# Performance work log

Hardware: AMD Instinct MI355X
Metric: run time of the kernel (lower is better)

Reference implementation:

```python
import jax, jax.numpy as jnp
import numpy as np

N_NODES = 50000
IN_CH = 128
OUT_CH = 64
HEADS = 2
N_EDGES = 400000
NEG_SLOPE = 0.2  # PyG GATConv default


def _glorot(key, shape):
    fan_in, fan_out = shape[0], shape[-1]
    lim = jnp.sqrt(6.0 / (fan_in + fan_out))
    return jax.random.uniform(key, shape, jnp.float32, -lim, lim)


def setup_inputs() -> dict:
    key = jax.random.key(0)
    ks = jax.random.split(key, 12)
    hid = 2 * OUT_CH  # per-head channels of conv1
    inp = {
        "x": jax.random.normal(ks[0], (N_NODES, IN_CH), jnp.float32),
        "edge_index": jax.random.randint(ks[1], (2, N_EDGES), 0, N_NODES, jnp.int32),
        # conv1: in=IN_CH, out=hid per head, HEADS heads, concat
        "W1": _glorot(ks[2], (IN_CH, HEADS * hid)),
        "att_src1": _glorot(ks[3], (HEADS, hid)),
        "att_dst1": _glorot(ks[4], (HEADS, hid)),
        "b1": jnp.zeros((HEADS * hid,), jnp.float32),
        # conv_mu: in=hid*HEADS, out=OUT_CH, 1 head
        "W_mu": _glorot(ks[5], (hid * HEADS, OUT_CH)),
        "att_src_mu": _glorot(ks[6], (1, OUT_CH)),
        "att_dst_mu": _glorot(ks[7], (1, OUT_CH)),
        "b_mu": jnp.zeros((OUT_CH,), jnp.float32),
        # conv_logstd: same shapes as conv_mu
        "W_ls": _glorot(ks[8], (hid * HEADS, OUT_CH)),
        "att_src_ls": _glorot(ks[9], (1, OUT_CH)),
        "att_dst_ls": _glorot(ks[10], (1, OUT_CH)),
        "b_ls": jnp.zeros((OUT_CH,), jnp.float32),
    }
    return inp


def gat_conv(x, src, dst, W, att_src, att_dst, b, n_nodes):
    """PyG GATConv (add_self_loops handled by caller in src/dst)."""
    H, C = att_src.shape
    h = (x @ W).reshape(n_nodes, H, C)                       # [N,H,C]
    a_src = jnp.einsum('nhc,hc->nh', h, att_src)             # [N,H]
    a_dst = jnp.einsum('nhc,hc->nh', h, att_dst)
    e = jax.nn.leaky_relu(a_src[src] + a_dst[dst], NEG_SLOPE)  # [E,H]
    # scatter-softmax over incoming edges per destination node
    m = jax.ops.segment_max(e, dst, num_segments=n_nodes)
    e = jnp.exp(e - m[dst])
    denom = jax.ops.segment_sum(e, dst, num_segments=n_nodes)
    alpha = e / (denom[dst] + 1e-16)                          # [E,H]
    out = jax.ops.segment_sum(h[src] * alpha[:, :, None], dst,
                              num_segments=n_nodes)           # [N,H,C]
    return out.reshape(n_nodes, H * C) + b


def reference(x, edge_index, W1, att_src1, att_dst1, b1,
              W_mu, att_src_mu, att_dst_mu, b_mu,
              W_ls, att_src_ls, att_dst_ls, b_ls):
    n = x.shape[0]
    loop = jnp.arange(n, dtype=edge_index.dtype)
    src = jnp.concatenate([edge_index[0], loop])  # add self-loops (PyG default)
    dst = jnp.concatenate([edge_index[1], loop])
    h = jax.nn.elu(gat_conv(x, src, dst, W1, att_src1, att_dst1, b1, n))
    mu = gat_conv(h, src, dst, W_mu, att_src_mu, att_dst_mu, b_mu, n)
    logstd = gat_conv(h, src, dst, W_ls, att_src_ls, att_dst_ls, b_ls, n)
    return (mu, logstd)
```

## Files before the change

kernel.cpp:

```cpp
#include <hip/hip_runtime.h>
#include <math.h>

#define N_NODES 50000
#define N_EDGES 400000
#define PAD 64

typedef __attribute__((ext_vector_type(8))) short bf16x8;
typedef __attribute__((ext_vector_type(4))) float f32x4;

__device__ __forceinline__ float lrelu(float x){ return x > 0.f ? x : 0.2f*x; }
__device__ __forceinline__ float bf2f(unsigned short u){ return __uint_as_float(((unsigned int)u)<<16); }
__device__ __forceinline__ unsigned short f2bf(float f){
    unsigned int b = __float_as_uint(f);
    return (unsigned short)((b + 0x7FFFu + ((b>>16)&1u)) >> 16);
}
__device__ __forceinline__ float4 bf4(ushort4 u){
    return make_float4(bf2f(u.x), bf2f(u.y), bf2f(u.z), bf2f(u.w));
}
__device__ __forceinline__ float wexp(float e){ return __expf(fminf(e, 80.f)); }

__global__ __launch_bounds__(256) void vprep_k(const float* __restrict__ W1,
        const float* __restrict__ attS, const float* __restrict__ attD,
        float* __restrict__ V1){
    int t = threadIdx.x;
    for (int idx = t; idx < 512; idx += 256){
        int v = idx >> 7, k = idx & 127;
        int h = v & 1;
        const float* attp = (v >> 1) ? attD : attS;
        float s = 0.f;
        #pragma unroll 8
        for (int c = 0; c < 128; c++)
            s = fmaf(W1[k*256 + h*128 + c], attp[h*128 + c], s);
        V1[idx] = s;
    }
}

__global__ __launch_bounds__(256) void prep_k(const float* __restrict__ x, unsigned short* __restrict__ xb,
        const float* __restrict__ V1, float2* __restrict__ as1, float2* __restrict__ ad1,
        const float* __restrict__ W1, const float* __restrict__ Wmu, const float* __restrict__ Wls,
        unsigned short* __restrict__ W1T, unsigned short* __restrict__ WmlT,
        const int* __restrict__ src, const int* __restrict__ dst,
        int* __restrict__ counts, int* __restrict__ csr_src){
    int t = threadIdx.x;
    int gthr = blockIdx.x*256 + t;

    int n = blockIdx.x*4 + (t >> 6);
    int lane = t & 63;
    if (n < N_NODES){
        int c0 = lane*2;
        float2 xv = ((const float2*)(x + (size_t)n*128))[lane];
        ((ushort2*)(xb + (size_t)n*128))[lane] = make_ushort2(f2bf(xv.x), f2bf(xv.y));
        float s0 = xv.x*V1[      c0] + xv.y*V1[      c0+1];
        float s1 = xv.x*V1[128 + c0] + xv.y*V1[128 + c0+1];
        float d0 = xv.x*V1[256 + c0] + xv.y*V1[256 + c0+1];
        float d1 = xv.x*V1[384 + c0] + xv.y*V1[384 + c0+1];
        #pragma unroll
        for (int m = 1; m < 64; m <<= 1){
            s0 += __shfl_xor(s0, m);
            s1 += __shfl_xor(s1, m);
            d0 += __shfl_xor(d0, m);
            d1 += __shfl_xor(d1, m);
        }
        if (lane == 0){
            as1[n] = make_float2(s0, s1);
            ad1[n] = make_float2(d0, d1);
        }
    }

    if (gthr < 32768){
        int i = gthr;
        int nn = i >> 7, k = i & 127;
        W1T[i] = f2bf(W1[k*256 + nn]);
        int n2 = i >> 8, k2 = i & 255;
        float v = (n2 < 64) ? Wmu[k2*64 + n2] : Wls[k2*64 + (n2-64)];
        WmlT[i] = f2bf(v);
    }

    if (gthr < N_EDGES){
        int d = dst[gthr];
        int pos = atomicAdd(&counts[d], 1);
        csr_src[d*PAD + pos] = src[gthr];
    }
}

__global__ __launch_bounds__(256) void agg1x_k(const unsigned short* __restrict__ xb,
        const float2* __restrict__ as, const float2* __restrict__ ad,
        const int* __restrict__ counts, const int* __restrict__ csr_src,
        unsigned short* __restrict__ aggx0, unsigned short* __restrict__ aggx1){
    int wave = threadIdx.x >> 6, lane = threadIdx.x & 63;
    int n = blockIdx.x*4 + wave;
    if (n >= N_NODES) return;

    float2 adn = ad[n], asn = as[n];
    float w0s = wexp(lrelu(asn.x + adn.x));
    float w1s = wexp(lrelu(asn.y + adn.y));
    float l0 = w0s, l1 = w1s;

    ushort2 u = ((const ushort2*)(xb + (size_t)n*128))[lane];
    float rx = bf2f(u.x), ry = bf2f(u.y);
    float a0x = w0s*rx, a0y = w0s*ry;
    float a1x = w1s*rx, a1y = w1s*ry;

    int deg = counts[n];
    int off = n*PAD;
    int dm1 = deg - 1;
    for (int k = 0; k < deg; k += 4){
        int s0 = csr_src[off + k];
        int s1 = csr_src[off + min(k+1, dm1)];
        int s2 = csr_src[off + min(k+2, dm1)];
        int s3 = csr_src[off + min(k+3, dm1)];
        float2 e0 = as[s0], e1 = as[s1], e2 = as[s2], e3 = as[s3];
        ushort2 u0 = ((const ushort2*)(xb + (size_t)s0*128))[lane];
        ushort2 u1 = ((const ushort2*)(xb + (size_t)s1*128))[lane];
        ushort2 u2 = ((const ushort2*)(xb + (size_t)s2*128))[lane];
        ushort2 u3 = ((const ushort2*)(xb + (size_t)s3*128))[lane];
        float w00 = wexp(lrelu(e0.x + adn.x));
        float w01 = wexp(lrelu(e0.y + adn.y));
        float w10 = (k+1 <= dm1) ? wexp(lrelu(e1.x + adn.x)) : 0.f;
        float w11 = (k+1 <= dm1) ? wexp(lrelu(e1.y + adn.y)) : 0.f;
        float w20 = (k+2 <= dm1) ? wexp(lrelu(e2.x + adn.x)) : 0.f;
        float w21 = (k+2 <= dm1) ? wexp(lrelu(e2.y + adn.y)) : 0.f;
        float w30 = (k+3 <= dm1) ? wexp(lrelu(e3.x + adn.x)) : 0.f;
        float w31 = (k+3 <= dm1) ? wexp(lrelu(e3.y + adn.y)) : 0.f;
        l0 += (w00 + w10) + (w20 + w30);
        l1 += (w01 + w11) + (w21 + w31);
        float r0x = bf2f(u0.x), r0y = bf2f(u0.y);
        float r1x = bf2f(u1.x), r1y = bf2f(u1.y);
        float r2x = bf2f(u2.x), r2y = bf2f(u2.y);
        float r3x = bf2f(u3.x), r3y = bf2f(u3.y);
        a0x = fmaf(w00, r0x, a0x); a0y = fmaf(w00, r0y, a0y);
        a1x = fmaf(w01, r0x, a1x); a1y = fmaf(w01, r0y, a1y);
        a0x = fmaf(w10, r1x, a0x); a0y = fmaf(w10, r1y, a0y);
        a1x = fmaf(w11, r1x, a1x); a1y = fmaf(w11, r1y, a1y);
        a0x = fmaf(w20, r2x, a0x); a0y = fmaf(w20, r2y, a0y);
        a1x = fmaf(w21, r2x, a1x); a1y = fmaf(w21, r2y, a1y);
        a0x = fmaf(w30, r3x, a0x); a0y = fmaf(w30, r3y, a0y);
        a1x = fmaf(w31, r3x, a1x); a1y = fmaf(w31, r3y, a1y);
    }

    float i0 = 1.f / (l0 + 1e-16f);
    float i1 = 1.f / (l1 + 1e-16f);
    ((ushort2*)(aggx0 + (size_t)n*128))[lane] = make_ushort2(f2bf(a0x*i0), f2bf(a0y*i0));
    ((ushort2*)(aggx1 + (size_t)n*128))[lane] = make_ushort2(f2bf(a1x*i1), f2bf(a1y*i1));
}

template<int MODE>
__global__ __launch_bounds__(256) void mfma_gemm_k(const unsigned short* __restrict__ A0,
        const unsigned short* __restrict__ A1,
        const unsigned short* __restrict__ BT, unsigned short* __restrict__ C,
        int M, int K, int ldc, const float* __restrict__ bias,
        const float* __restrict__ attS0, const float* __restrict__ attD0,
        const float* __restrict__ attS1, const float* __restrict__ attD1,
        float* __restrict__ outS, float* __restrict__ outD){
    __shared__ unsigned short As[128*40];
    __shared__ unsigned short Bs[128*40];
    int t = threadIdx.x;
    int lane = t & 63, wid = t >> 6;
    int wy = wid >> 1, wx = wid & 1;
    int quad = lane >> 4, l15 = lane & 15;
    int row0 = blockIdx.y * 128;
    int col0 = blockIdx.x * 128;
    const unsigned short* A = (MODE == 0 && blockIdx.x) ? A1 : A0;

    f32x4 acc[4][4];
    #pragma unroll
    for (int i = 0; i < 4; i++)
        #pragma unroll
        for (int j = 0; j < 4; j++)
            acc[i][j] = (f32x4){0.f, 0.f, 0.f, 0.f};

    int r = t >> 2;
    int cofs = (t & 3) * 8;

    for (int k0 = 0; k0 < K; k0 += 32){
        int gr0 = min(row0 + r,      M-1);
        int gr1 = min(row0 + r + 64, M-1);
        float4 av0 = *(const float4*)(A  + (size_t)gr0*K + k0 + cofs);
        float4 av1 = *(const float4*)(A  + (size_t)gr1*K + k0 + cofs);
        float4 bv0 = *(const float4*)(BT + (size_t)(col0 + r)*K      + k0 + cofs);
        float4 bv1 = *(const float4*)(BT + (size_t)(col0 + r + 64)*K + k0 + cofs);
        __syncthreads();
        *(float4*)&As[r*40 + cofs]      = av0;
        *(float4*)&As[(r+64)*40 + cofs] = av1;
        *(float4*)&Bs[r*40 + cofs]      = bv0;
        *(float4*)&Bs[(r+64)*40 + cofs] = bv1;
        __syncthreads();

        bf16x8 af[4], bf[4];
        #pragma unroll
        for (int i = 0; i < 4; i++)
            af[i] = *(const bf16x8*)&As[(wy*64 + i*16 + l15)*40 + quad*8];
        #pragma unroll
        for (int j = 0; j < 4; j++)
            bf[j] = *(const bf16x8*)&Bs[(wx*64 + j*16 + l15)*40 + quad*8];
        #pragma unroll
        for (int i = 0; i < 4; i++)
            #pragma unroll
            for (int j = 0; j < 4; j++)
                acc[i][j] = __builtin_amdgcn_mfma_f32_16x16x32_bf16(af[i], bf[j], acc[i][j], 0, 0, 0);
    }

    float aS[4], aD[4], bvals[4];
    #pragma unroll
    for (int j = 0; j < 4; j++){
        int cc = col0 + wx*64 + j*16 + l15;
        if (MODE == 0){
            bvals[j] = bias[cc];
        } else {
            int c2 = j*16 + l15;
            aS[j] = wx ? attS1[c2] : attS0[c2];
            aD[j] = wx ? attD1[c2] : attD0[c2];
        }
    }

    #pragma unroll
    for (int i = 0; i < 4; i++){
        #pragma unroll
        for (int reg = 0; reg < 4; reg++){
            int rr = row0 + wy*64 + i*16 + quad*4 + reg;
            if (MODE == 0){
                if (rr < M){
                    #pragma unroll
                    for (int j = 0; j < 4; j++){
                        int cc = col0 + wx*64 + j*16 + l15;
                        float v = acc[i][j][reg] + bvals[j];
                        v = v > 0.f ? v : __expf(v) - 1.f;
                        C[(size_t)rr*ldc + cc] = f2bf(v);
                    }
                }
            } else {
                float sp = 0.f, dp = 0.f;
                #pragma unroll
                for (int j = 0; j < 4; j++){
                    float v = acc[i][j][reg];
                    int cc = col0 + wx*64 + j*16 + l15;
                    if (rr < M) C[(size_t)rr*ldc + cc] = f2bf(v);
                    sp = fmaf(v, aS[j], sp);
                    dp = fmaf(v, aD[j], dp);
                }
                #pragma unroll
                for (int msk = 1; msk < 16; msk <<= 1){
                    sp += __shfl_xor(sp, msk);
                    dp += __shfl_xor(dp, msk);
                }
                if (l15 == 0 && rr < M){
                    outS[rr*2 + wx] = sp;
                    outD[rr*2 + wx] = dp;
                }
            }
        }
    }
}

__global__ __launch_bounds__(256) void agg2_k(const unsigned short* __restrict__ hml,
        const float* __restrict__ as, const float* __restrict__ ad,
        const int* __restrict__ counts, const int* __restrict__ csr_src,
        const float* __restrict__ b_mu, const float* __restrict__ b_ls,
        float* __restrict__ out){
    int grp = threadIdx.x >> 5, lane = threadIdx.x & 31;
    int n = blockIdx.x*8 + grp;
    if (n >= N_NODES) return;
    int g = lane >> 4;
    const ushort4* hv = (const ushort4*)hml;

    float adh = ad[n*2 + g];
    float ash = as[n*2 + g];

    float w = wexp(lrelu(ash + adh));
    float l = w;
    float4 r = bf4(hv[(size_t)n*32 + lane]);
    float4 acc = make_float4(w*r.x, w*r.y, w*r.z, w*r.w);

    int deg = counts[n];
    int off = n*PAD;
    int dm1 = deg - 1;
    for (int k = 0; k < deg; k += 4){
        int s0 = csr_src[off + k];
        int s1 = csr_src[off + min(k+1, dm1)];
        int s2 = csr_src[off + min(k+2, dm1)];
        int s3 = csr_src[off + min(k+3, dm1)];
        float e0 = as[s0*2 + g], e1 = as[s1*2 + g];
        float e2 = as[s2*2 + g], e3 = as[s3*2 + g];
        float4 r0 = bf4(hv[(size_t)s0*32 + lane]);
        float4 r1 = bf4(hv[(size_t)s1*32 + lane]);
        float4 r2 = bf4(hv[(size_t)s2*32 + lane]);
        float4 r3 = bf4(hv[(size_t)s3*32 + lane]);
        float w0 = wexp(lrelu(e0 + adh));
        float w1 = (k+1 <= dm1) ? wexp(lrelu(e1 + adh)) : 0.f;
        float w2 = (k+2 <= dm1) ? wexp(lrelu(e2 + adh)) : 0.f;
        float w3 = (k+3 <= dm1) ? wexp(lrelu(e3 + adh)) : 0.f;
        l += (w0 + w1) + (w2 + w3);
        acc.x = fmaf(w0, r0.x, acc.x); acc.x = fmaf(w1, r1.x, acc.x);
        acc.x = fmaf(w2, r2.x, acc.x); acc.x = fmaf(w3, r3.x, acc.x);
        acc.y = fmaf(w0, r0.y, acc.y); acc.y = fmaf(w1, r1.y, acc.y);
        acc.y = fmaf(w2, r2.y, acc.y); acc.y = fmaf(w3, r3.y, acc.y);
        acc.z = fmaf(w0, r0.z, acc.z); acc.z = fmaf(w1, r1.z, acc.z);
        acc.z = fmaf(w2, r2.z, acc.z); acc.z = fmaf(w3, r3.z, acc.z);
        acc.w = fmaf(w0, r0.w, acc.w); acc.w = fmaf(w1, r1.w, acc.w);
        acc.w = fmaf(w2, r2.w, acc.w); acc.w = fmaf(w3, r3.w, acc.w);
    }

    float invl = 1.f / (l + 1e-16f);
    int c = (lane & 15) * 4;
    const float* bb = g ? b_ls : b_mu;
    float4 b4 = *(const float4*)&bb[c];
    float4 v;
    v.x = acc.x*invl + b4.x; v.y = acc.y*invl + b4.y;
    v.z = acc.z*invl + b4.z; v.w = acc.w*invl + b4.w;
    float* base = g ? (out + (size_t)N_NODES*64) : out;
    *(float4*)&base[(size_t)n*64 + c] = v;
}

extern "C" void kernel_launch(void* const* d_in, const int* in_sizes, int n_in,
                              void* d_out, int out_size, void* d_ws, size_t ws_size,
                              hipStream_t stream) {
    const float* x           = (const float*)d_in[0];
    const int*   ei          = (const int*)d_in[1];
    const float* W1          = (const float*)d_in[2];
    const float* att_src1    = (const float*)d_in[3];
    const float* att_dst1    = (const float*)d_in[4];
    const float* b1          = (const float*)d_in[5];
    const float* W_mu        = (const float*)d_in[6];
    const float* att_src_mu  = (const float*)d_in[7];
    const float* att_dst_mu  = (const float*)d_in[8];
    const float* b_mu        = (const float*)d_in[9];
    const float* W_ls        = (const float*)d_in[10];
    const float* att_src_ls  = (const float*)d_in[11];
    const float* att_dst_ls  = (const float*)d_in[12];
    const float* b_ls        = (const float*)d_in[13];
    float* out = (float*)d_out;

    const int* srcp = ei;
    const int* dstp = ei + N_EDGES;

    unsigned short* xb    = (unsigned short*)d_ws;
    unsigned short* aggx0 = xb    + (size_t)N_NODES*128;
    unsigned short* aggx1 = aggx0 + (size_t)N_NODES*128;
    unsigned short* hbuf  = aggx1 + (size_t)N_NODES*128;
    unsigned short* hml   = hbuf  + (size_t)N_NODES*256;
    unsigned short* W1T   = hml   + (size_t)N_NODES*128;
    unsigned short* WmlT  = W1T   + 32768;
    int*   counts = (int*)(WmlT + 32768);
    float2* as1   = (float2*)(counts + N_NODES);
    float2* ad1   = as1 + N_NODES;
    float*  as2   = (float*)(ad1 + N_NODES);
    float*  ad2   = as2 + 2*N_NODES;
    float*  V1    = ad2 + 2*N_NODES;
    int*    csr   = (int*)(V1 + 512);

    hipMemsetAsync(counts, 0, N_NODES*sizeof(int), stream);

    vprep_k<<<1, 256, 0, stream>>>(W1, att_src1, att_dst1, V1);

    prep_k<<<12500, 256, 0, stream>>>(x, xb, V1, as1, ad1, W1, W_mu, W_ls, W1T, WmlT,
                                      srcp, dstp, counts, csr);

    agg1x_k<<<(N_NODES + 3) / 4, 256, 0, stream>>>(xb, as1, ad1, counts, csr, aggx0, aggx1);

    mfma_gemm_k<0><<<dim3(2, 391), 256, 0, stream>>>(aggx0, aggx1, W1T, hbuf, N_NODES, 128, 256,
                                                     b1, nullptr, nullptr, nullptr, nullptr,
                                                     nullptr, nullptr);

    mfma_gemm_k<2><<<dim3(1, 391), 256, 0, stream>>>(hbuf, hbuf, WmlT, hml, N_NODES, 256, 128,
                                                     nullptr, att_src_mu, att_dst_mu,
                                                     att_src_ls, att_dst_ls, as2, ad2);

    agg2_k<<<(N_NODES + 7) / 8, 256, 0, stream>>>(hml, as2, ad2, counts, csr, b_mu, b_ls, out);
}
```

Baseline: 231.4 us.

## Fuse both GEMMs via LDS-resident hidden tile and merge setup kernels

The first-layer GEMM (with bias and ELU) and the second-layer mu/logstd GEMM now run in one kernel per 128-row tile. The ELU output is kept as a bf16 tile in shared memory instead of being written to and re-read from a global hbuf. The memset, the attention-vector precompute and the weight transposes move into one init kernel. The x-prep kernel now handles one node per 32 lanes with float4 loads. This cuts global traffic and launch count, but the larger shared-memory footprint lowers occupancy, and each GEMM block now runs three sequential GEMM phases over only 391 blocks.

New measurement: 233.1 us. Within noise of the previous version (+0.7%).

```diff
diff --git a/kernel.cpp b/kernel.cpp
--- a/kernel.cpp
+++ b/kernel.cpp
@@ -19,61 +19,60 @@
 }
 __device__ __forceinline__ float wexp(float e){ return __expf(fminf(e, 80.f)); }
 
-__global__ __launch_bounds__(256) void vprep_k(const float* __restrict__ W1,
+__global__ __launch_bounds__(256) void init_k(const float* __restrict__ W1,
+        const float* __restrict__ Wmu, const float* __restrict__ Wls,
         const float* __restrict__ attS, const float* __restrict__ attD,
-        float* __restrict__ V1){
-    int t = threadIdx.x;
-    for (int idx = t; idx < 512; idx += 256){
-        int v = idx >> 7, k = idx & 127;
-        int h = v & 1;
-        const float* attp = (v >> 1) ? attD : attS;
-        float s = 0.f;
-        #pragma unroll 8
-        for (int c = 0; c < 128; c++)
-            s = fmaf(W1[k*256 + h*128 + c], attp[h*128 + c], s);
-        V1[idx] = s;
-    }
-}
-
-__global__ __launch_bounds__(256) void prep_k(const float* __restrict__ x, unsigned short* __restrict__ xb,
-        const float* __restrict__ V1, float2* __restrict__ as1, float2* __restrict__ ad1,
-        const float* __restrict__ W1, const float* __restrict__ Wmu, const float* __restrict__ Wls,
         unsigned short* __restrict__ W1T, unsigned short* __restrict__ WmlT,
-        const int* __restrict__ src, const int* __restrict__ dst,
-        int* __restrict__ counts, int* __restrict__ csr_src){
-    int t = threadIdx.x;
-    int gthr = blockIdx.x*256 + t;
-
-    int n = blockIdx.x*4 + (t >> 6);
-    int lane = t & 63;
-    if (n < N_NODES){
-        int c0 = lane*2;
-        float2 xv = ((const float2*)(x + (size_t)n*128))[lane];
-        ((ushort2*)(xb + (size_t)n*128))[lane] = make_ushort2(f2bf(xv.x), f2bf(xv.y));
-        float s0 = xv.x*V1[      c0] + xv.y*V1[      c0+1];
-        float s1 = xv.x*V1[128 + c0] + xv.y*V1[128 + c0+1];
-        float d0 = xv.x*V1[256 + c0] + xv.y*V1[256 + c0+1];
-        float d1 = xv.x*V1[384 + c0] + xv.y*V1[384 + c0+1];
-        #pragma unroll
-        for (int m = 1; m < 64; m <<= 1){
-            s0 += __shfl_xor(s0, m);
-            s1 += __shfl_xor(s1, m);
-            d0 += __shfl_xor(d0, m);
-            d1 += __shfl_xor(d1, m);
-        }
-        if (lane == 0){
-            as1[n] = make_float2(s0, s1);
-            ad1[n] = make_float2(d0, d1);
-        }
-    }
-
-    if (gthr < 32768){
-        int i = gthr;
+        float* __restrict__ V1, int* __restrict__ counts){
+    int i = blockIdx.x*256 + threadIdx.x;
+    if (i < N_NODES) counts[i] = 0;
+    if (i < 32768){
         int nn = i >> 7, k = i & 127;
         W1T[i] = f2bf(W1[k*256 + nn]);
         int n2 = i >> 8, k2 = i & 255;
         float v = (n2 < 64) ? Wmu[k2*64 + n2] : Wls[k2*64 + (n2-64)];
         WmlT[i] = f2bf(v);
+    }
+    if (blockIdx.x == 0){
+        for (int idx = threadIdx.x; idx < 512; idx += 256){
+            int v = idx >> 7, k = idx & 127;
+            int h = v & 1;
+            const float* attp = (v >> 1) ? attD : attS;
+            float s = 0.f;
+            #pragma unroll 8
+            for (int c = 0; c < 128; c++)
+                s = fmaf(W1[k*256 + h*128 + c], attp[h*128 + c], s);
+            V1[idx] = s;
+        }
+    }
+}
+
+__global__ __launch_bounds__(256) void prep_k(const float* __restrict__ x, unsigned short* __restrict__ xb,
+        const float* __restrict__ V1, float2* __restrict__ as1, float2* __restrict__ ad1,
+        const int* __restrict__ src, const int* __restrict__ dst,
+        int* __restrict__ counts, int* __restrict__ csr_src){
+    int t = threadIdx.x;
+    int gthr = blockIdx.x*256 + t;
+    int n = blockIdx.x*8 + (t >> 5);
+    int lane = t & 31;
+
+    float4 xv = ((const float4*)(x + (size_t)n*128))[lane];
+    ((ushort4*)(xb + (size_t)n*128))[lane] = make_ushort4(f2bf(xv.x), f2bf(xv.y), f2bf(xv.z), f2bf(xv.w));
+    int c0 = lane*4;
+    float s0 = xv.x*V1[      c0] + xv.y*V1[      c0+1] + xv.z*V1[      c0+2] + xv.w*V1[      c0+3];
+    float s1 = xv.x*V1[128 + c0] + xv.y*V1[128 + c0+1] + xv.z*V1[128 + c0+2] + xv.w*V1[128 + c0+3];
+    float d0 = xv.x*V1[256 + c0] + xv.y*V1[256 + c0+1] + xv.z*V1[256 + c0+2] + xv.w*V1[256 + c0+3];
+    float d1 = xv.x*V1[384 + c0] + xv.y*V1[384 + c0+1] + xv.z*V1[384 + c0+2] + xv.w*V1[384 + c0+3];
+    #pragma unroll
+    for (int m = 1; m < 32; m <<= 1){
+        s0 += __shfl_xor(s0, m, 32);
+        s1 += __shfl_xor(s1, m, 32);
+        d0 += __shfl_xor(d0, m, 32);
+        d1 += __shfl_xor(d1, m, 32);
+    }
+    if (lane == 0){
+        as1[n] = make_float2(s0, s1);
+        ad1[n] = make_float2(d0, d1);
     }
 
     if (gthr < N_EDGES){
@@ -144,44 +143,87 @@
     ((ushort2*)(aggx1 + (size_t)n*128))[lane] = make_ushort2(f2bf(a1x*i1), f2bf(a1y*i1));
 }
 
-template<int MODE>
-__global__ __launch_bounds__(256) void mfma_gemm_k(const unsigned short* __restrict__ A0,
-        const unsigned short* __restrict__ A1,
-        const unsigned short* __restrict__ BT, unsigned short* __restrict__ C,
-        int M, int K, int ldc, const float* __restrict__ bias,
-        const float* __restrict__ attS0, const float* __restrict__ attD0,
-        const float* __restrict__ attS1, const float* __restrict__ attD1,
-        float* __restrict__ outS, float* __restrict__ outD){
+__global__ __launch_bounds__(256) void gemm12_k(const unsigned short* __restrict__ aggx0,
+        const unsigned short* __restrict__ aggx1,
+        const unsigned short* __restrict__ W1T, const unsigned short* __restrict__ WmlT,
+        const float* __restrict__ b1, unsigned short* __restrict__ hml,
+        const float* __restrict__ attSmu, const float* __restrict__ attDmu,
+        const float* __restrict__ attSls, const float* __restrict__ attDls,
+        float* __restrict__ as2, float* __restrict__ ad2, int M){
     __shared__ unsigned short As[128*40];
     __shared__ unsigned short Bs[128*40];
+    __shared__ unsigned short Ht[128*264];
     int t = threadIdx.x;
     int lane = t & 63, wid = t >> 6;
     int wy = wid >> 1, wx = wid & 1;
     int quad = lane >> 4, l15 = lane & 15;
-    int row0 = blockIdx.y * 128;
-    int col0 = blockIdx.x * 128;
-    const unsigned short* A = (MODE == 0 && blockIdx.x) ? A1 : A0;
+    int row0 = blockIdx.x * 128;
+    int r = t >> 2, cofs = (t & 3) * 8;
 
     f32x4 acc[4][4];
+
+    for (int h = 0; h < 2; h++){
+        const unsigned short* A = h ? aggx1 : aggx0;
+        #pragma unroll
+        for (int i = 0; i < 4; i++)
+            #pragma unroll
+            for (int j = 0; j < 4; j++)
+                acc[i][j] = (f32x4){0.f, 0.f, 0.f, 0.f};
+
+        for (int k0 = 0; k0 < 128; k0 += 32){
+            int gr0 = min(row0 + r,      M-1);
+            int gr1 = min(row0 + r + 64, M-1);
+            float4 av0 = *(const float4*)(A   + (size_t)gr0*128 + k0 + cofs);
+            float4 av1 = *(const float4*)(A   + (size_t)gr1*128 + k0 + cofs);
+            float4 bv0 = *(const float4*)(W1T + (size_t)(h*128 + r)*128      + k0 + cofs);
+            float4 bv1 = *(const float4*)(W1T + (size_t)(h*128 + r + 64)*128 + k0 + cofs);
+            __syncthreads();
+            *(float4*)&As[r*40 + cofs]      = av0;
+            *(float4*)&As[(r+64)*40 + cofs] = av1;
+            *(float4*)&Bs[r*40 + cofs]      = bv0;
+            *(float4*)&Bs[(r+64)*40 + cofs] = bv1;
+            __syncthreads();
+
+            bf16x8 af[4], bf[4];
+            #pragma unroll
+            for (int i = 0; i < 4; i++)
+                af[i] = *(const bf16x8*)&As[(wy*64 + i*16 + l15)*40 + quad*8];
+            #pragma unroll
+            for (int j = 0; j < 4; j++)
+                bf[j] = *(const bf16x8*)&Bs[(wx*64 + j*16 + l15)*40 + quad*8];
+            #pragma unroll
+            for (int i = 0; i < 4; i++)
+                #pragma unroll
+                for (int j = 0; j < 4; j++)
+                    acc[i][j] = __builtin_amdgcn_mfma_f32_16x16x32_bf16(af[i], bf[j], acc[i][j], 0, 0, 0);
+        }
+
+        #pragma unroll
+        for (int i = 0; i < 4; i++){
+            #pragma unroll
+            for (int reg = 0; reg < 4; reg++){
+                int lr = wy*64 + i*16 + quad*4 + reg;
+                #pragma unroll
+                for (int j = 0; j < 4; j++){
+                    int cc = h*128 + wx*64 + j*16 + l15;
+                    float v = acc[i][j][reg] + b1[cc];
+                    v = v > 0.f ? v : __expf(v) - 1.f;
+                    Ht[lr*264 + cc] = f2bf(v);
+                }
+            }
+        }
+    }
+
     #pragma unroll
     for (int i = 0; i < 4; i++)
         #pragma unroll
         for (int j = 0; j < 4; j++)
             acc[i][j] = (f32x4){0.f, 0.f, 0.f, 0.f};
 
-    int r = t >> 2;
-    int cofs = (t & 3) * 8;
-
-    for (int k0 = 0; k0 < K; k0 += 32){
-        int gr0 = min(row0 + r,      M-1);
-        int gr1 = min(row0 + r + 64, M-1);
-        float4 av0 = *(const float4*)(A  + (size_t)gr0*K + k0 + cofs);
-        float4 av1 = *(const float4*)(A  + (size_t)gr1*K + k0 + cofs);
-        float4 bv0 = *(const float4*)(BT + (size_t)(col0 + r)*K      + k0 + cofs);
-        float4 bv1 = *(const float4*)(BT + (size_t)(col0 + r + 64)*K + k0 + cofs);
+    for (int k0 = 0; k0 < 256; k0 += 32){
+        float4 bv0 = *(const float4*)(WmlT + (size_t)r*256        + k0 + cofs);
+        float4 bv1 = *(const float4*)(WmlT + (size_t)(r + 64)*256 + k0 + cofs);
         __syncthreads();
-        *(float4*)&As[r*40 + cofs]      = av0;
-        *(float4*)&As[(r+64)*40 + cofs] = av1;
         *(float4*)&Bs[r*40 + cofs]      = bv0;
         *(float4*)&Bs[(r+64)*40 + cofs] = bv1;
         __syncthreads();
@@ -189,7 +231,7 @@
         bf16x8 af[4], bf[4];
         #pragma unroll
         for (int i = 0; i < 4; i++)
-            af[i] = *(const bf16x8*)&As[(wy*64 + i*16 + l15)*40 + quad*8];
+            af[i] = *(const bf16x8*)&Ht[(wy*64 + i*16 + l15)*264 + k0 + quad*8];
         #pragma unroll
         for (int j = 0; j < 4; j++)
             bf[j] = *(const bf16x8*)&Bs[(wx*64 + j*16 + l15)*40 + quad*8];
@@ -200,17 +242,12 @@
                 acc[i][j] = __builtin_amdgcn_mfma_f32_16x16x32_bf16(af[i], bf[j], acc[i][j], 0, 0, 0);
     }
 
-    float aS[4], aD[4], bvals[4];
+    float aS[4], aD[4];
     #pragma unroll
     for (int j = 0; j < 4; j++){
-        int cc = col0 + wx*64 + j*16 + l15;
-        if (MODE == 0){
-            bvals[j] = bias[cc];
-        } else {
-            int c2 = j*16 + l15;
-            aS[j] = wx ? attS1[c2] : attS0[c2];
-            aD[j] = wx ? attD1[c2] : attD0[c2];
-        }
+        int c2 = j*16 + l15;
+        aS[j] = wx ? attSls[c2] : attSmu[c2];
+        aD[j] = wx ? attDls[c2] : attDmu[c2];
     }
 
     #pragma unroll
@@ -218,35 +255,23 @@
         #pragma unroll
         for (int reg = 0; reg < 4; reg++){
             int rr = row0 + wy*64 + i*16 + quad*4 + reg;
-            if (MODE == 0){
-                if (rr < M){
-                    #pragma unroll
-                    for (int j = 0; j < 4; j++){
-                        int cc = col0 + wx*64 + j*16 + l15;
-                        float v = acc[i][j][reg] + bvals[j];
-                        v = v > 0.f ? v : __expf(v) - 1.f;
-                        C[(size_t)rr*ldc + cc] = f2bf(v);
-                    }
-                }
-            } else {
-                float sp = 0.f, dp = 0.f;
-                #pragma unroll
-                for (int j = 0; j < 4; j++){
-                    float v = acc[i][j][reg];
-                    int cc = col0 + wx*64 + j*16 + l15;
-                    if (rr < M) C[(size_t)rr*ldc + cc] = f2bf(v);
-                    sp = fmaf(v, aS[j], sp);
-                    dp = fmaf(v, aD[j], dp);
-                }
-                #pragma unroll
-                for (int msk = 1; msk < 16; msk <<= 1){
-                    sp += __shfl_xor(sp, msk);
-                    dp += __shfl_xor(dp, msk);
-                }
-                if (l15 == 0 && rr < M){
-                    outS[rr*2 + wx] = sp;
-                    outD[rr*2 + wx] = dp;
-                }
+            float sp = 0.f, dp = 0.f;
+            #pragma unroll
+            for (int j = 0; j < 4; j++){
+                float v = acc[i][j][reg];
+                int cc = wx*64 + j*16 + l15;
+                if (rr < M) hml[(size_t)rr*128 + cc] = f2bf(v);
+                sp = fmaf(v, aS[j], sp);
+                dp = fmaf(v, aD[j], dp);
+            }
+            #pragma unroll
+            for (int msk = 1; msk < 16; msk <<= 1){
+                sp += __shfl_xor(sp, msk);
+                dp += __shfl_xor(dp, msk);
+            }
+            if (l15 == 0 && rr < M){
+                as2[rr*2 + wx] = sp;
+                ad2[rr*2 + wx] = dp;
             }
         }
     }
@@ -336,8 +361,7 @@
     unsigned short* xb    = (unsigned short*)d_ws;
     unsigned short* aggx0 = xb    + (size_t)N_NODES*128;
     unsigned short* aggx1 = aggx0 + (size_t)N_NODES*128;
-    unsigned short* hbuf  = aggx1 + (size_t)N_NODES*128;
-    unsigned short* hml   = hbuf  + (size_t)N_NODES*256;
+    unsigned short* hml   = aggx1 + (size_t)N_NODES*128;
     unsigned short* W1T   = hml   + (size_t)N_NODES*128;
     unsigned short* WmlT  = W1T   + 32768;
     int*   counts = (int*)(WmlT + 32768);
@@ -348,22 +372,15 @@
     float*  V1    = ad2 + 2*N_NODES;
     int*    csr   = (int*)(V1 + 512);
 
-    hipMemsetAsync(counts, 0, N_NODES*sizeof(int), stream);
-
-    vprep_k<<<1, 256, 0, stream>>>(W1, att_src1, att_dst1, V1);
-
-    prep_k<<<12500, 256, 0, stream>>>(x, xb, V1, as1, ad1, W1, W_mu, W_ls, W1T, WmlT,
-                                      srcp, dstp, counts, csr);
+    init_k<<<196, 256, 0, stream>>>(W1, W_mu, W_ls, att_src1, att_dst1, W1T, WmlT, V1, counts);
+
+    prep_k<<<6250, 256, 0, stream>>>(x, xb, V1, as1, ad1, srcp, dstp, counts, csr);
 
     agg1x_k<<<(N_NODES + 3) / 4, 256, 0, stream>>>(xb, as1, ad1, counts, csr, aggx0, aggx1);
 
-    mfma_gemm_k<0><<<dim3(2, 391), 256, 0, stream>>>(aggx0, aggx1, W1T, hbuf, N_NODES, 128, 256,
-                                                     b1, nullptr, nullptr, nullptr, nullptr,
-                                                     nullptr, nullptr);
-
-    mfma_gemm_k<2><<<dim3(1, 391), 256, 0, stream>>>(hbuf, hbuf, WmlT, hml, N_NODES, 256, 128,
-                                                     nullptr, att_src_mu, att_dst_mu,
-                                                     att_src_ls, att_dst_ls, as2, ad2);
+    gemm12_k<<<391, 256, 0, stream>>>(aggx0, aggx1, W1T, WmlT, b1, hml,
+                                      att_src_mu, att_dst_mu, att_src_ls, att_dst_ls,
+                                      as2, ad2, N_NODES);
 
     agg2_k<<<(N_NODES + 7) / 8, 256, 0, stream>>>(hml, as2, ad2, counts, csr, b_mu, b_ls, out);
 }
```
